# Optimization experiments

Measured on AMD Instinct MI355X. Metric: run time of the kernel, lower is better.

The kernel has to match this reference:

```python
import math
import jax, jax.numpy as jnp
import numpy as np

B, LD, LS = 1, 512, 2048
C_S, C_H, H, PQ, PV = 384, 16, 12, 4, 8
EPS, INF = 1e-08, 1e9


def _quat_to_rot(q):
    q = q / jnp.linalg.norm(q, axis=-1, keepdims=True)
    w, x, y, z = q[..., 0], q[..., 1], q[..., 2], q[..., 3]
    R = jnp.stack([
        1 - 2 * (y * y + z * z), 2 * (x * y - w * z), 2 * (x * z + w * y),
        2 * (x * y + w * z), 1 - 2 * (x * x + z * z), 2 * (y * z - w * x),
        2 * (x * z - w * y), 2 * (y * z + w * x), 1 - 2 * (x * x + y * y)],
        axis=-1)
    return R.reshape(q.shape[:-1] + (3, 3))


def setup_inputs() -> dict:
    key = jax.random.key(0)
    ks = jax.random.split(key, 14)
    s_dst = jax.random.normal(ks[0], (B, LD, C_S), jnp.float32)
    s_src = jax.random.normal(ks[1], (B, LS, C_S), jnp.float32)
    R_dst = _quat_to_rot(jax.random.normal(ks[2], (B, LD, 4), jnp.float32))
    t_dst = jax.random.normal(ks[3], (B, LD, 3), jnp.float32) * 3.0
    R_src = _quat_to_rot(jax.random.normal(ks[4], (B, LS, 4), jnp.float32))
    t_src = jax.random.normal(ks[5], (B, LS, 3), jnp.float32) * 3.0
    dst_mask = jnp.ones((B, LD), jnp.float32)
    src_mask = (jax.random.uniform(ks[6], (B, LS)) < 0.9).astype(jnp.float32)
    sc = 0.02
    W_q = jax.random.normal(ks[7], (C_S, H * C_H), jnp.float32) * sc
    W_kv = jax.random.normal(ks[8], (C_S, 2 * H * C_H), jnp.float32) * sc
    W_qp = jax.random.normal(ks[9], (C_S, H * PQ * 3), jnp.float32) * sc
    W_kvp = jax.random.normal(ks[10], (C_S, H * (PQ + PV) * 3), jnp.float32) * sc
    W_out = jax.random.normal(ks[11], (H * (C_H + PV * 4), C_S), jnp.float32) * sc
    b_out = jnp.zeros((C_S,), jnp.float32)
    # ipa_point_weights_init_: softplus^-1(1) = log(e - 1)
    head_w = jnp.full((H,), float(np.log(np.e - 1.0)), jnp.float32)
    return dict(s_dst=s_dst, s_src=s_src, R_dst=R_dst, t_dst=t_dst,
                R_src=R_src, t_src=t_src, dst_mask=dst_mask, src_mask=src_mask,
                W_q=W_q, W_kv=W_kv, W_qp=W_qp, W_kvp=W_kvp,
                W_out=W_out, b_out=b_out, head_w=head_w)


def _split3_stack(x):
    # torch.split into 3 chunks on last dim then stack(dim=-1): [..., 3n] -> [..., n, 3]
    b, l, c3 = x.shape
    return jnp.moveaxis(x.reshape(b, l, 3, c3 // 3), -2, -1)


def _ipa_forward(s_dst, s_src, R_dst, t_dst, R_src, t_src, dst_mask, src_mask,
                 W_q, W_kv, W_qp, W_kvp, W_out, b_out, head_w):
    b, ld, _ = s_dst.shape
    ls = s_src.shape[1]
    gmask = (dst_mask[:, None, :, None] * src_mask[:, None, None, :])  # [B,1,Ld,Ls]

    q = (s_dst @ W_q).reshape(b, ld, H, C_H)
    kv = (s_src @ W_kv).reshape(b, ls, H, 2 * C_H)
    k, v = kv[..., :C_H], kv[..., C_H:]

    # points in global frame
    qp = _split3_stack(s_dst @ W_qp)                     # [B,Ld,H*PQ,3] local
    qp = jnp.einsum('blij,blpj->blpi', R_dst, qp) + t_dst[:, :, None, :]
    qp = qp.reshape(b, ld, H, PQ, 3)
    kvp = _split3_stack(s_src @ W_kvp)                   # [B,Ls,H*(PQ+PV),3]
    kvp = jnp.einsum('blij,blpj->blpi', R_src, kvp) + t_src[:, :, None, :]
    kvp = kvp.reshape(b, ls, H, PQ + PV, 3)
    k_pts, v_pts = kvp[..., :PQ, :], kvp[..., PQ:, :]

    # scalar attention scores
    a = jnp.einsum('bihc,bjhc->bhij', q, k) * math.sqrt(1.0 / (2 * C_H))
    a_sd = a * gmask

    # point attention: squared distances of global-frame points
    diff = qp[:, :, None, :, :, :] - k_pts[:, None, :, :, :, :]   # [B,Ld,Ls,H,PQ,3]
    pt2 = jnp.sum(diff * diff, axis=-1)                           # [B,Ld,Ls,H,PQ]
    hw = jax.nn.softplus(head_w) * math.sqrt(1.0 / (2 * (PQ * 9.0 / 2)))
    pt_att = jnp.sum(pt2 * hw[None, None, None, :, None], axis=-1) * (-0.5)
    pt_att = jnp.transpose(pt_att, (0, 3, 1, 2))                  # [B,H,Ld,Ls]
    a_pts = pt_att * gmask

    sq_mask = INF * (dst_mask[:, :, None] * src_mask[:, None, :] - 1.0)
    a = jax.nn.softmax(a + pt_att + sq_mask[:, None, :, :], axis=-1)

    # scalar value aggregation
    o = jnp.einsum('bhij,bjhc->bihc', a, v).reshape(b, ld, H * C_H)
    # point value aggregation, then back to dst local frame
    o_pt = jnp.einsum('bhij,bjhpc->bihpc', a, v_pts)              # [B,Ld,H,PV,3]
    o_pt = jnp.einsum('bikj,bihpk->bihpj', R_dst,
                      o_pt - t_dst[:, :, None, None, :])
    o_pt_norm = jnp.sqrt(jnp.sum(o_pt ** 2, axis=-1) + EPS).reshape(b, ld, H * PV)
    o_pt_flat = o_pt.reshape(b, ld, H * PV, 3)

    cat = jnp.concatenate([o, o_pt_flat[..., 0], o_pt_flat[..., 1],
                           o_pt_flat[..., 2], o_pt_norm], axis=-1)
    s_upd = cat @ W_out + b_out
    return s_upd, a, a_sd, a_pts


def reference(s_dst, s_src, R_dst, t_dst, R_src, t_src, dst_mask, src_mask,
              W_q, W_kv, W_qp, W_kvp, W_out, b_out, head_w):
    return _ipa_forward(s_dst, s_src, R_dst, t_dst, R_src, t_src,
                        dst_mask, src_mask, W_q, W_kv, W_qp, W_kvp,
                        W_out, b_out, head_w)
```

## Files before the change

kernel.cpp:

```cpp
#include <hip/hip_runtime.h>
#include <hip/hip_bf16.h>

#define LD 512
#define LS 2048
#define CS 384
#define CH 16
#define NH 12
#define PQ 4
#define PV 8
#define QCW 336
#define KVW 816

typedef __bf16 bf16x8 __attribute__((ext_vector_type(8)));
typedef float  f32x4  __attribute__((ext_vector_type(4)));

__device__ inline void split_frag(const float* __restrict__ p, bf16x8& hi, bf16x8& lo)
{
    float4 x = *(const float4*)p;
    float4 y = *(const float4*)(p + 4);
    float f[8] = {x.x, x.y, x.z, x.w, y.x, y.y, y.z, y.w};
#pragma unroll
    for (int e = 0; e < 8; ++e) {
        __bf16 h = (__bf16)f[e];
        hi[e] = h;
        lo[e] = (__bf16)(f[e] - (float)h);
    }
}

__global__ __launch_bounds__(256) void transpose_w_all_kernel(
    const float* __restrict__ W_q, const float* __restrict__ W_kv,
    const float* __restrict__ W_qp, const float* __restrict__ W_kvp,
    const float* __restrict__ W_out,
    float* __restrict__ Wt_qc, float* __restrict__ Wt_kvc,
    float* __restrict__ Wt_out)
{
    int b = blockIdx.x;
    const float* src; float* dst; int R, Cc, gx;
    if (b < 72)       {         src = W_q;   dst = Wt_qc;             R = 384; Cc = 192; gx = 12; }
    else if (b < 132) { b -= 72;  src = W_qp;  dst = Wt_qc + 192*384; R = 384; Cc = 144; gx = 12; }
    else if (b < 276) { b -= 132; src = W_kv;  dst = Wt_kvc;          R = 384; Cc = 384; gx = 12; }
    else if (b < 444) { b -= 276; src = W_kvp; dst = Wt_kvc + 384*384;R = 384; Cc = 432; gx = 12; }
    else              { b -= 444; src = W_out; dst = Wt_out;          R = 576; Cc = 384; gx = 18; }
    const int r0 = (b % gx) * 32, c0 = (b / gx) * 32;

    __shared__ float tile[32][33];
    const int tx = threadIdx.x & 31, ty = threadIdx.x >> 5;
#pragma unroll
    for (int rr = 0; rr < 32; rr += 8) {
        int r = r0 + ty + rr, c = c0 + tx;
        tile[ty + rr][tx] = (r < R && c < Cc) ? src[(size_t)r * Cc + c] : 0.f;
    }
    __syncthreads();
#pragma unroll
    for (int rr = 0; rr < 32; rr += 8) {
        int c = c0 + ty + rr, r = r0 + tx;
        if (c < Cc && r < R) dst[(size_t)c * R + r] = tile[tx][ty + rr];
    }
}

__global__ __launch_bounds__(64) void mfma_gemm_bt_kernel(
    const float* __restrict__ A, const float* __restrict__ Bt,
    const float* __restrict__ bias, float* __restrict__ C,
    int M, int N, int K)
{
    const int m0 = blockIdx.x * 32;
    const int n0 = blockIdx.y * 32;
    const int lane = threadIdx.x;
    const int row16 = lane & 15, kq = lane >> 4;

    const float* ap0 = A + (size_t)(m0 + row16) * K + kq * 8;
    const float* ap1 = ap0 + (size_t)16 * K;
    const float* bp0 = Bt + (size_t)(n0 + row16) * K + kq * 8;
    const float* bp1 = bp0 + (size_t)16 * K;
    const bool n1ok = (n0 + 16) < N;

    f32x4 acc00 = {0.f, 0.f, 0.f, 0.f};
    f32x4 acc10 = {0.f, 0.f, 0.f, 0.f};
    f32x4 acc01 = {0.f, 0.f, 0.f, 0.f};
    f32x4 acc11 = {0.f, 0.f, 0.f, 0.f};

    for (int k = 0; k < K; k += 32) {
        bf16x8 a0h, a0l, a1h, a1l, b0h, b0l, b1h, b1l;
        split_frag(ap0 + k, a0h, a0l);
        split_frag(ap1 + k, a1h, a1l);
        split_frag(bp0 + k, b0h, b0l);
        acc00 = __builtin_amdgcn_mfma_f32_16x16x32_bf16(a0h, b0h, acc00, 0, 0, 0);
        acc00 = __builtin_amdgcn_mfma_f32_16x16x32_bf16(a0h, b0l, acc00, 0, 0, 0);
        acc00 = __builtin_amdgcn_mfma_f32_16x16x32_bf16(a0l, b0h, acc00, 0, 0, 0);
        acc10 = __builtin_amdgcn_mfma_f32_16x16x32_bf16(a1h, b0h, acc10, 0, 0, 0);
        acc10 = __builtin_amdgcn_mfma_f32_16x16x32_bf16(a1h, b0l, acc10, 0, 0, 0);
        acc10 = __builtin_amdgcn_mfma_f32_16x16x32_bf16(a1l, b0h, acc10, 0, 0, 0);
        if (n1ok) {
            split_frag(bp1 + k, b1h, b1l);
            acc01 = __builtin_amdgcn_mfma_f32_16x16x32_bf16(a0h, b1h, acc01, 0, 0, 0);
            acc01 = __builtin_amdgcn_mfma_f32_16x16x32_bf16(a0h, b1l, acc01, 0, 0, 0);
            acc01 = __builtin_amdgcn_mfma_f32_16x16x32_bf16(a0l, b1h, acc01, 0, 0, 0);
            acc11 = __builtin_amdgcn_mfma_f32_16x16x32_bf16(a1h, b1h, acc11, 0, 0, 0);
            acc11 = __builtin_amdgcn_mfma_f32_16x16x32_bf16(a1h, b1l, acc11, 0, 0, 0);
            acc11 = __builtin_amdgcn_mfma_f32_16x16x32_bf16(a1l, b1h, acc11, 0, 0, 0);
        }
    }

    const float bv0 = bias ? bias[n0 + row16] : 0.f;
    const float bv1 = (bias && n1ok) ? bias[n0 + 16 + row16] : 0.f;
#pragma unroll
    for (int r = 0; r < 4; ++r) {
        const int mA = m0 + kq * 4 + r;
        const int mB = mA + 16;
        C[(size_t)mA * N + n0 + row16] = acc00[r] + bv0;
        C[(size_t)mB * N + n0 + row16] = acc10[r] + bv0;
        if (n1ok) {
            C[(size_t)mA * N + n0 + 16 + row16] = acc01[r] + bv1;
            C[(size_t)mB * N + n0 + 16 + row16] = acc11[r] + bv1;
        }
    }
}

__global__ __launch_bounds__(256) void prep_kernel(
    const float* __restrict__ qcat, const float* __restrict__ kvcat,
    const float* __restrict__ Rd, const float* __restrict__ td,
    const float* __restrict__ Rs, const float* __restrict__ ts,
    float* __restrict__ qp_rot, float* __restrict__ sqq,
    float* __restrict__ kT, float* __restrict__ vAllT,
    float* __restrict__ kpT, float* __restrict__ sqkT)
{
    const int t = threadIdx.x;
    if (blockIdx.y < NH) {
        const int h = blockIdx.y, j0 = blockIdx.x * 64;
        __shared__ float tile[64][33];
        __shared__ float ot[36][64];
        __shared__ float nrm[64][4];
        __shared__ float rt[64][12];

#pragma unroll
        for (int s = 0; s < 3; ++s) {
            int ld = t + s * 256;
            int jl = ld / 12, q = ld % 12;
            rt[jl][q] = (q < 9) ? Rs[(size_t)(j0 + jl) * 9 + q]
                                : ts[(size_t)(j0 + jl) * 3 + (q - 9)];
        }
#pragma unroll
        for (int r = 0; r < 2; ++r) {
            int f = t + r * 256;
            int jl = f >> 3, c4 = (f & 7) * 4;
            float4 v = *(const float4*)(kvcat + (size_t)(j0 + jl) * KVW + h * 32 + c4);
            tile[jl][c4 + 0] = v.x;
            tile[jl][c4 + 1] = v.y;
            tile[jl][c4 + 2] = v.z;
            tile[jl][c4 + 3] = v.w;
        }
        __syncthreads();

        {
            const int jl = t & 63, cr = t >> 6;
#pragma unroll
            for (int cg = 0; cg < 8; ++cg) {
                int c = cg * 4 + cr;
                float v = tile[jl][c];
                if (c < 16) kT[((size_t)h * 16 + c) * LS + j0 + jl] = v;
                else        vAllT[((size_t)h * 40 + (c - 16)) * LS + j0 + jl] = v;
            }
        }

#pragma unroll
        for (int s = 0; s < 3; ++s) {
            int u = t + s * 256;
            int jl = u / 12, p = u % 12;
            const float* src = kvcat + (size_t)(j0 + jl) * KVW + 384 + h * 12 + p;
            float x = src[0], y = src[144], z = src[288];
            const float* R = &rt[jl][0];
            float rx = R[0] * x + R[1] * y + R[2] * z + R[9];
            float ry = R[3] * x + R[4] * y + R[5] * z + R[10];
            float rz = R[6] * x + R[7] * y + R[8] * z + R[11];
            if (p < 4) {
                ot[p * 3 + 0][jl] = rx;
                ot[p * 3 + 1][jl] = ry;
                ot[p * 3 + 2][jl] = rz;
                nrm[jl][p] = rx * rx + ry * ry + rz * rz;
            } else {
                int r0 = 12 + (p - 4) * 3;
                ot[r0 + 0][jl] = rx;
                ot[r0 + 1][jl] = ry;
                ot[r0 + 2][jl] = rz;
            }
        }
        __syncthreads();

#pragma unroll
        for (int w = 0; w < 9; ++w) {
            int idx = t + w * 256;
            int row = idx >> 6, jl = idx & 63;
            float v = ot[row][jl];
            if (row < 12) kpT[((size_t)h * 12 + row) * LS + j0 + jl] = v;
            else          vAllT[((size_t)h * 40 + 16 + (row - 12)) * LS + j0 + jl] = v;
        }
        if (t < 64)
            sqkT[(size_t)h * LS + j0 + t] = nrm[t][0] + nrm[t][1] + nrm[t][2] + nrm[t][3];
    } else {
        const int i0 = blockIdx.x * 16;
        __shared__ float part[16][48];
        __shared__ float rtd[16][12];
        if (t < 192) {
            int il = t / 12, q = t % 12;
            rtd[il][q] = (q < 9) ? Rd[(size_t)(i0 + il) * 9 + q]
                                 : td[(size_t)(i0 + il) * 3 + (q - 9)];
        }
        __syncthreads();
#pragma unroll
        for (int s = 0; s < 3; ++s) {
            int u = t + s * 256;
            int il = u / 48, pt = u % 48;
            int i = i0 + il;
            float x = qcat[(size_t)i * QCW + 192 + pt];
            float y = qcat[(size_t)i * QCW + 240 + pt];
            float z = qcat[(size_t)i * QCW + 288 + pt];
            const float* R = &rtd[il][0];
            float rx = R[0] * x + R[1] * y + R[2] * z + R[9];
            float ry = R[3] * x + R[4] * y + R[5] * z + R[10];
            float rz = R[6] * x + R[7] * y + R[8] * z + R[11];
            qp_rot[(size_t)i * 144 + pt * 3 + 0] = rx;
            qp_rot[(size_t)i * 144 + pt * 3 + 1] = ry;
            qp_rot[(size_t)i * 144 + pt * 3 + 2] = rz;
            part[il][pt] = rx * rx + ry * ry + rz * rz;
        }
        __syncthreads();
        if (t < 192) {
            int il = t / 12, hh = t % 12;
            sqq[(size_t)(i0 + il) * NH + hh] =
                part[il][hh * 4] + part[il][hh * 4 + 1] +
                part[il][hh * 4 + 2] + part[il][hh * 4 + 3];
        }
    }
}

__global__ __launch_bounds__(256) void score_softmax_kernel(
    const float* __restrict__ qb, const float* __restrict__ kT,
    const float* __restrict__ qpb, const float* __restrict__ kpT,
    const float* __restrict__ sqq_g, const float* __restrict__ sqkT,
    const float* __restrict__ dmask, const float* __restrict__ smask,
    const float* __restrict__ head_w,
    float* __restrict__ a_out, float* __restrict__ asd_out,
    float* __restrict__ apts_out)
{
    const int h = blockIdx.y;
    const int i0 = blockIdx.x * 4;
    const int t = threadIdx.x;

    __shared__ float qs[4][32];
    __shared__ float sqq_s[4];
    __shared__ float dm_s[4];
    __shared__ float red[4][4];

    if (t < 128) {
        int i = t >> 5, c = t & 31;
        float v = 0.f;
        if (c < 16)      v = qb[(size_t)(i0 + i) * QCW + h * CH + c];
        else if (c < 28) v = qpb[(size_t)(i0 + i) * 144 + h * 12 + (c - 16)];
        qs[i][c] = v;
    } else if (t < 132) {
        int i = t - 128;
        sqq_s[i] = sqq_g[(size_t)(i0 + i) * NH + h];
        dm_s[i] = dmask[i0 + i];
    }
    const float hwv = log1pf(__expf(head_w[h])) * (1.0f / 6.0f);
    const float s1 = 0.17677669529663687f;
    const size_t rowbase = ((size_t)h * LD + i0) * LS;
    __syncthreads();

    float4 sregv[4][2];
    float mx[4] = {-3.0e38f, -3.0e38f, -3.0e38f, -3.0e38f};

#pragma unroll
    for (int jc = 0; jc < 2; ++jc) {
        const int j = (jc * 256 + t) * 4;
        float4 sm4 = *(const float4*)(smask + j);
        float4 sqk4 = *(const float4*)(sqkT + (size_t)h * LS + j);

        float4 kk[16];
#pragma unroll
        for (int c = 0; c < 16; ++c)
            kk[c] = *(const float4*)(kT + ((size_t)h * 16 + c) * LS + j);

        float4 qk4[4];
#pragma unroll
        for (int i = 0; i < 4; ++i) {
            const float4* q4 = (const float4*)&qs[i][0];
            float4 q0 = q4[0], q1 = q4[1], q2 = q4[2], q3 = q4[3];
            float4 a;
            a.x = q0.x * kk[0].x + q0.y * kk[1].x + q0.z * kk[2].x + q0.w * kk[3].x
                + q1.x * kk[4].x + q1.y * kk[5].x + q1.z * kk[6].x + q1.w * kk[7].x
                + q2.x * kk[8].x + q2.y * kk[9].x + q2.z * kk[10].x + q2.w * kk[11].x
                + q3.x * kk[12].x + q3.y * kk[13].x + q3.z * kk[14].x + q3.w * kk[15].x;
            a.y = q0.x * kk[0].y + q0.y * kk[1].y + q0.z * kk[2].y + q0.w * kk[3].y
                + q1.x * kk[4].y + q1.y * kk[5].y + q1.z * kk[6].y + q1.w * kk[7].y
                + q2.x * kk[8].y + q2.y * kk[9].y + q2.z * kk[10].y + q2.w * kk[11].y
                + q3.x * kk[12].y + q3.y * kk[13].y + q3.z * kk[14].y + q3.w * kk[15].y;
            a.z = q0.x * kk[0].z + q0.y * kk[1].z + q0.z * kk[2].z + q0.w * kk[3].z
                + q1.x * kk[4].z + q1.y * kk[5].z + q1.z * kk[6].z + q1.w * kk[7].z
                + q2.x * kk[8].z + q2.y * kk[9].z + q2.z * kk[10].z + q2.w * kk[11].z
                + q3.x * kk[12].z + q3.y * kk[13].z + q3.z * kk[14].z + q3.w * kk[15].z;
            a.w = q0.x * kk[0].w + q0.y * kk[1].w + q0.z * kk[2].w + q0.w * kk[3].w
                + q1.x * kk[4].w + q1.y * kk[5].w + q1.z * kk[6].w + q1.w * kk[7].w
                + q2.x * kk[8].w + q2.y * kk[9].w + q2.z * kk[10].w + q2.w * kk[11].w
                + q3.x * kk[12].w + q3.y * kk[13].w + q3.z * kk[14].w + q3.w * kk[15].w;
            qk4[i] = a;
        }

        float4 pp[12];
#pragma unroll
        for (int d = 0; d < 12; ++d)
            pp[d] = *(const float4*)(kpT + ((size_t)h * 12 + d) * LS + j);

        float4 dp4[4];
#pragma unroll
        for (int i = 0; i < 4; ++i) {
            const float4* r4 = (const float4*)&qs[i][16];
            float4 r0 = r4[0], r1 = r4[1], r2 = r4[2];
            float4 d;
            d.x = r0.x * pp[0].x + r0.y * pp[1].x + r0.z * pp[2].x + r0.w * pp[3].x
                + r1.x * pp[4].x + r1.y * pp[5].x + r1.z * pp[6].x + r1.w * pp[7].x
                + r2.x * pp[8].x + r2.y * pp[9].x + r2.z * pp[10].x + r2.w * pp[11].x;
            d.y = r0.x * pp[0].y + r0.y * pp[1].y + r0.z * pp[2].y + r0.w * pp[3].y
                + r1.x * pp[4].y + r1.y * pp[5].y + r1.z * pp[6].y + r1.w * pp[7].y
                + r2.x * pp[8].y + r2.y * pp[9].y + r2.z * pp[10].y + r2.w * pp[11].y;
            d.z = r0.x * pp[0].z + r0.y * pp[1].z + r0.z * pp[2].z + r0.w * pp[3].z
                + r1.x * pp[4].z + r1.y * pp[5].z + r1.z * pp[6].z + r1.w * pp[7].z
                + r2.x * pp[8].z + r2.y * pp[9].z + r2.z * pp[10].z + r2.w * pp[11].z;
            d.w = r0.x * pp[0].w + r0.y * pp[1].w + r0.z * pp[2].w + r0.w * pp[3].w
                + r1.x * pp[4].w + r1.y * pp[5].w + r1.z * pp[6].w + r1.w * pp[7].w
                + r2.x * pp[8].w + r2.y * pp[9].w + r2.z * pp[10].w + r2.w * pp[11].w;
            dp4[i] = d;
        }

#pragma unroll
        for (int i = 0; i < 4; ++i) {
            float sqq = sqq_s[i];
            float dm = dm_s[i];
            float4 qk, pt, g, logit;
            qk.x = qk4[i].x * s1; qk.y = qk4[i].y * s1;
            qk.z = qk4[i].z * s1; qk.w = qk4[i].w * s1;
            pt.x = -0.5f * hwv * (sqq + sqk4.x - 2.f * dp4[i].x);
            pt.y = -0.5f * hwv * (sqq + sqk4.y - 2.f * dp4[i].y);
            pt.z = -0.5f * hwv * (sqq + sqk4.z - 2.f * dp4[i].z);
            pt.w = -0.5f * hwv * (sqq + sqk4.w - 2.f * dp4[i].w);
            g.x = dm * sm4.x; g.y = dm * sm4.y; g.z = dm * sm4.z; g.w = dm * sm4.w;
            size_t idx = rowbase + (size_t)i * LS + j;
            f32x4 asd = {qk.x * g.x, qk.y * g.y, qk.z * g.z, qk.w * g.w};
            f32x4 apts = {pt.x * g.x, pt.y * g.y, pt.z * g.z, pt.w * g.w};
            __builtin_nontemporal_store(asd, (f32x4*)(asd_out + idx));
            __builtin_nontemporal_store(apts, (f32x4*)(apts_out + idx));
            logit.x = qk.x + pt.x + 1.0e9f * (g.x - 1.0f);
            logit.y = qk.y + pt.y + 1.0e9f * (g.y - 1.0f);
            logit.z = qk.z + pt.z + 1.0e9f * (g.z - 1.0f);
            logit.w = qk.w + pt.w + 1.0e9f * (g.w - 1.0f);
            sregv[i][jc] = logit;
            mx[i] = fmaxf(mx[i], fmaxf(fmaxf(logit.x, logit.y), fmaxf(logit.z, logit.w)));
        }
    }

    const int lane = t & 63, wid = t >> 6;
#pragma unroll
    for (int i = 0; i < 4; ++i) {
        float v = mx[i];
        for (int off = 32; off > 0; off >>= 1) v = fmaxf(v, __shfl_xor(v, off));
        if (lane == 0) red[wid][i] = v;
    }
    __syncthreads();
    float M[4], sum[4] = {0.f, 0.f, 0.f, 0.f};
#pragma unroll
    for (int i = 0; i < 4; ++i)
        M[i] = fmaxf(fmaxf(red[0][i], red[1][i]), fmaxf(red[2][i], red[3][i]));
    __syncthreads();

#pragma unroll
    for (int jc = 0; jc < 2; ++jc) {
#pragma unroll
        for (int i = 0; i < 4; ++i) {
            float4 e;
            e.x = __expf(sregv[i][jc].x - M[i]);
            e.y = __expf(sregv[i][jc].y - M[i]);
            e.z = __expf(sregv[i][jc].z - M[i]);
            e.w = __expf(sregv[i][jc].w - M[i]);
            sregv[i][jc] = e;
            sum[i] += e.x + e.y + e.z + e.w;
        }
    }
#pragma unroll
    for (int i = 0; i < 4; ++i) {
        float v = sum[i];
        for (int off = 32; off > 0; off >>= 1) v += __shfl_xor(v, off);
        if (lane == 0) red[wid][i] = v;
    }
    __syncthreads();
    float inv[4];
#pragma unroll
    for (int i = 0; i < 4; ++i)
        inv[i] = 1.0f / (red[0][i] + red[1][i] + red[2][i] + red[3][i]);

#pragma unroll
    for (int jc = 0; jc < 2; ++jc) {
        const int j = (jc * 256 + t) * 4;
#pragma unroll
        for (int i = 0; i < 4; ++i) {
            float4 e = sregv[i][jc];
            float4 o = make_float4(e.x * inv[i], e.y * inv[i], e.z * inv[i], e.w * inv[i]);
            *(float4*)(a_out + rowbase + (size_t)i * LS + j) = o;
        }
    }
}

__global__ __launch_bounds__(512) void av_mfma_kernel(
    const float* __restrict__ a, const float* __restrict__ vAllT,
    float* __restrict__ o_buf, float* __restrict__ opt_buf)
{
    const int m0 = blockIdx.x * 16;
    const int h  = blockIdx.y;
    const int t = threadIdx.x;
    const int lane = t & 63;
    const int wid  = t >> 6;
    const int row16 = lane & 15, kq = lane >> 4;

    const size_t kbase = (size_t)wid * 256 + kq * 8;
    const float* ap  = a     + ((size_t)h * LD + m0 + row16) * LS + kbase;
    const float* v0p = vAllT + ((size_t)h * 40 +  0 + row16) * LS + kbase;
    const float* v1p = vAllT + ((size_t)h * 40 + 16 + row16) * LS + kbase;
    const float* v2p = vAllT + ((size_t)h * 40 + 24 + row16) * LS + kbase;

    f32x4 acc0 = {0.f, 0.f, 0.f, 0.f};
    f32x4 acc1 = {0.f, 0.f, 0.f, 0.f};
    f32x4 acc2 = {0.f, 0.f, 0.f, 0.f};

#pragma unroll 2
    for (int kk = 0; kk < 256; kk += 32) {
        bf16x8 ah, al, bh, bl;
        split_frag(ap + kk, ah, al);

        split_frag(v0p + kk, bh, bl);
        acc0 = __builtin_amdgcn_mfma_f32_16x16x32_bf16(ah, bh, acc0, 0, 0, 0);
        acc0 = __builtin_amdgcn_mfma_f32_16x16x32_bf16(ah, bl, acc0, 0, 0, 0);
        acc0 = __builtin_amdgcn_mfma_f32_16x16x32_bf16(al, bh, acc0, 0, 0, 0);

        split_frag(v1p + kk, bh, bl);
        acc1 = __builtin_amdgcn_mfma_f32_16x16x32_bf16(ah, bh, acc1, 0, 0, 0);
        acc1 = __builtin_amdgcn_mfma_f32_16x16x32_bf16(ah, bl, acc1, 0, 0, 0);
        acc1 = __builtin_amdgcn_mfma_f32_16x16x32_bf16(al, bh, acc1, 0, 0, 0);

        split_frag(v2p + kk, bh, bl);
        acc2 = __builtin_amdgcn_mfma_f32_16x16x32_bf16(ah, bh, acc2, 0, 0, 0);
        acc2 = __builtin_amdgcn_mfma_f32_16x16x32_bf16(ah, bl, acc2, 0, 0, 0);
        acc2 = __builtin_amdgcn_mfma_f32_16x16x32_bf16(al, bh, acc2, 0, 0, 0);
    }

    __shared__ float red[8][64][13];
#pragma unroll
    for (int r = 0; r < 4; ++r) {
        red[wid][lane][r]     = acc0[r];
        red[wid][lane][4 + r] = acc1[r];
        red[wid][lane][8 + r] = acc2[r];
    }
    __syncthreads();

    if (wid == 0) {
        float s[12];
#pragma unroll
        for (int r = 0; r < 12; ++r) {
            float v = red[0][lane][r];
#pragma unroll
            for (int w = 1; w < 8; ++w) v += red[w][lane][r];
            s[r] = v;
        }
        const int ib = m0 + kq * 4;
#pragma unroll
        for (int r = 0; r < 4; ++r) {
            const int i = ib + r;
            o_buf[(size_t)i * 192 + h * 16 + row16] = s[r];
            opt_buf[(size_t)i * 288 + h * 24 + row16] = s[4 + r];
            if (row16 >= 8)
                opt_buf[(size_t)i * 288 + h * 24 + 8 + row16] = s[8 + r];
        }
    }
}

__global__ __launch_bounds__(192) void finalize_kernel(
    const float* __restrict__ o_buf, const float* __restrict__ opt_buf,
    const float* __restrict__ Rd, const float* __restrict__ td,
    float* __restrict__ cat)
{
    const int i = blockIdx.x, t = threadIdx.x;
    cat[i * 576 + t] = o_buf[i * 192 + t];
    if (t < 96) {
        const float* op = opt_buf + i * 288 + t * 3;
        float x = op[0] - td[i * 3 + 0];
        float y = op[1] - td[i * 3 + 1];
        float z = op[2] - td[i * 3 + 2];
        const float* R = Rd + i * 9;
        float rx = R[0] * x + R[3] * y + R[6] * z;
        float ry = R[1] * x + R[4] * y + R[7] * z;
        float rz = R[2] * x + R[5] * y + R[8] * z;
        float* cc = cat + i * 576 + 192;
        cc[t] = rx;
        cc[96 + t] = ry;
        cc[192 + t] = rz;
        cc[288 + t] = sqrtf(rx * rx + ry * ry + rz * rz + 1e-8f);
    }
}

extern "C" void kernel_launch(void* const* d_in, const int* in_sizes, int n_in,
                              void* d_out, int out_size, void* d_ws, size_t ws_size,
                              hipStream_t stream)
{
    (void)in_sizes; (void)n_in; (void)out_size; (void)ws_size;
    const float* s_dst    = (const float*)d_in[0];
    const float* s_src    = (const float*)d_in[1];
    const float* R_dst    = (const float*)d_in[2];
    const float* t_dst    = (const float*)d_in[3];
    const float* R_src    = (const float*)d_in[4];
    const float* t_src    = (const float*)d_in[5];
    const float* dst_mask = (const float*)d_in[6];
    const float* src_mask = (const float*)d_in[7];
    const float* W_q      = (const float*)d_in[8];
    const float* W_kv     = (const float*)d_in[9];
    const float* W_qp     = (const float*)d_in[10];
    const float* W_kvp    = (const float*)d_in[11];
    const float* W_out    = (const float*)d_in[12];
    const float* b_out    = (const float*)d_in[13];
    const float* head_w   = (const float*)d_in[14];

    float* ws = (float*)d_ws;
    float* qcat    = ws;
    float* kvcat   = qcat    + 172032;
    float* qp_rot  = kvcat   + 1671168;
    float* sq_q    = qp_rot  + 73728;
    float* o_buf   = sq_q    + 6144;
    float* opt_buf = o_buf   + 98304;
    float* cat_buf = opt_buf + 147456;
    float* kT      = cat_buf + 294912;
    float* vAllT   = kT      + 393216;
    float* kpT     = vAllT   + 983040;
    float* sqkT    = kpT     + 294912;
    float* Wt_qc   = sqkT    + 24576;
    float* Wt_kvc  = Wt_qc   + 129024;
    float* Wt_out  = Wt_kvc  + 313344;

    float* out_s    = (float*)d_out;
    float* out_a    = out_s    + 196608;
    float* out_asd  = out_a    + 12582912;
    float* out_apts = out_asd  + 12582912;

    transpose_w_all_kernel<<<dim3(660), dim3(256), 0, stream>>>(
        W_q, W_kv, W_qp, W_kvp, W_out, Wt_qc, Wt_kvc, Wt_out);
    mfma_gemm_bt_kernel<<<dim3(16, 11), dim3(64), 0, stream>>>(s_dst, Wt_qc,  nullptr, qcat,  LD, QCW, CS);
    mfma_gemm_bt_kernel<<<dim3(64, 26), dim3(64), 0, stream>>>(s_src, Wt_kvc, nullptr, kvcat, LS, KVW, CS);
    prep_kernel<<<dim3(32, 13), dim3(256), 0, stream>>>(
        qcat, kvcat, R_dst, t_dst, R_src, t_src,
        qp_rot, sq_q, kT, vAllT, kpT, sqkT);
    score_softmax_kernel<<<dim3(LD / 4, NH), dim3(256), 0, stream>>>(
        qcat, kT, qp_rot, kpT, sq_q, sqkT, dst_mask, src_mask, head_w,
        out_a, out_asd, out_apts);
    av_mfma_kernel<<<dim3(LD / 16, NH), dim3(512), 0, stream>>>(out_a, vAllT, o_buf, opt_buf);
    finalize_kernel<<<LD, 192, 0, stream>>>(o_buf, opt_buf, R_dst, t_dst, cat_buf);
    mfma_gemm_bt_kernel<<<dim3(16, 12), dim3(64), 0, stream>>>(cat_buf, Wt_out, b_out, out_s, LD, CS, 576);
}
```

Before: 305.8 us.

## Drop weight transpose kernel; read weights directly in fused projection GEMM

Removes the separate weight-transpose launch and instead loads the untransposed W matrices with strided per-lane reads inside the GEMMs. The q and kv projection GEMMs are merged into one launch that picks its A, W and output by block index. This cuts two launches and an extra pass over the weights through memory. In exchange, the B-fragment loads become 8 scalar strided loads per lane instead of two float4 loads, which may hurt load efficiency, though adjacent lanes still read adjacent columns.

```diff
diff --git a/kernel.cpp b/kernel.cpp
--- a/kernel.cpp
+++ b/kernel.cpp
@@ -27,51 +27,48 @@
     }
 }
 
-__global__ __launch_bounds__(256) void transpose_w_all_kernel(
-    const float* __restrict__ W_q, const float* __restrict__ W_kv,
-    const float* __restrict__ W_qp, const float* __restrict__ W_kvp,
-    const float* __restrict__ W_out,
-    float* __restrict__ Wt_qc, float* __restrict__ Wt_kvc,
-    float* __restrict__ Wt_out)
-{
-    int b = blockIdx.x;
-    const float* src; float* dst; int R, Cc, gx;
-    if (b < 72)       {         src = W_q;   dst = Wt_qc;             R = 384; Cc = 192; gx = 12; }
-    else if (b < 132) { b -= 72;  src = W_qp;  dst = Wt_qc + 192*384; R = 384; Cc = 144; gx = 12; }
-    else if (b < 276) { b -= 132; src = W_kv;  dst = Wt_kvc;          R = 384; Cc = 384; gx = 12; }
-    else if (b < 444) { b -= 276; src = W_kvp; dst = Wt_kvc + 384*384;R = 384; Cc = 432; gx = 12; }
-    else              { b -= 444; src = W_out; dst = Wt_out;          R = 576; Cc = 384; gx = 18; }
-    const int r0 = (b % gx) * 32, c0 = (b / gx) * 32;
-
-    __shared__ float tile[32][33];
-    const int tx = threadIdx.x & 31, ty = threadIdx.x >> 5;
-#pragma unroll
-    for (int rr = 0; rr < 32; rr += 8) {
-        int r = r0 + ty + rr, c = c0 + tx;
-        tile[ty + rr][tx] = (r < R && c < Cc) ? src[(size_t)r * Cc + c] : 0.f;
-    }
-    __syncthreads();
-#pragma unroll
-    for (int rr = 0; rr < 32; rr += 8) {
-        int c = c0 + ty + rr, r = r0 + tx;
-        if (c < Cc && r < R) dst[(size_t)c * R + r] = tile[tx][ty + rr];
-    }
-}
-
-__global__ __launch_bounds__(64) void mfma_gemm_bt_kernel(
-    const float* __restrict__ A, const float* __restrict__ Bt,
-    const float* __restrict__ bias, float* __restrict__ C,
-    int M, int N, int K)
-{
-    const int m0 = blockIdx.x * 32;
-    const int n0 = blockIdx.y * 32;
+__device__ inline void split_frag_w(const float* __restrict__ Wp, int stride,
+                                    bf16x8& hi, bf16x8& lo)
+{
+    float f[8];
+#pragma unroll
+    for (int e = 0; e < 8; ++e) f[e] = Wp[(size_t)e * stride];
+#pragma unroll
+    for (int e = 0; e < 8; ++e) {
+        __bf16 h = (__bf16)f[e];
+        hi[e] = h;
+        lo[e] = (__bf16)(f[e] - (float)h);
+    }
+}
+
+__global__ __launch_bounds__(64) void proj_gemm_kernel(
+    const float* __restrict__ s_dst, const float* __restrict__ s_src,
+    const float* __restrict__ W_q, const float* __restrict__ W_qp,
+    const float* __restrict__ W_kv, const float* __restrict__ W_kvp,
+    float* __restrict__ qcat, float* __restrict__ kvcat)
+{
+    const float* A; float* C; int N, m0, n0, Nw; const float* Wsrc; int ncol0;
+    if (blockIdx.x < 176) {
+        int b = blockIdx.x;
+        A = s_dst; C = qcat; N = QCW;
+        m0 = (b & 15) * 32; n0 = (b >> 4) * 32;
+        if (n0 < 192) { Wsrc = W_q;  Nw = 192; ncol0 = n0; }
+        else          { Wsrc = W_qp; Nw = 144; ncol0 = n0 - 192; }
+    } else {
+        int b = blockIdx.x - 176;
+        A = s_src; C = kvcat; N = KVW;
+        m0 = (b & 63) * 32; n0 = (b >> 6) * 32;
+        if (n0 < 384) { Wsrc = W_kv;  Nw = 384; ncol0 = n0; }
+        else          { Wsrc = W_kvp; Nw = 432; ncol0 = n0 - 384; }
+    }
     const int lane = threadIdx.x;
     const int row16 = lane & 15, kq = lane >> 4;
+    const int K = CS;
 
     const float* ap0 = A + (size_t)(m0 + row16) * K + kq * 8;
     const float* ap1 = ap0 + (size_t)16 * K;
-    const float* bp0 = Bt + (size_t)(n0 + row16) * K + kq * 8;
-    const float* bp1 = bp0 + (size_t)16 * K;
+    const float* wp0 = Wsrc + (size_t)(kq * 8) * Nw + ncol0 + row16;
+    const float* wp1 = wp0 + 16;
     const bool n1ok = (n0 + 16) < N;
 
     f32x4 acc00 = {0.f, 0.f, 0.f, 0.f};
@@ -83,7 +80,7 @@
         bf16x8 a0h, a0l, a1h, a1l, b0h, b0l, b1h, b1l;
         split_frag(ap0 + k, a0h, a0l);
         split_frag(ap1 + k, a1h, a1l);
-        split_frag(bp0 + k, b0h, b0l);
+        split_frag_w(wp0 + (size_t)k * Nw, Nw, b0h, b0l);
         acc00 = __builtin_amdgcn_mfma_f32_16x16x32_bf16(a0h, b0h, acc00, 0, 0, 0);
         acc00 = __builtin_amdgcn_mfma_f32_16x16x32_bf16(a0h, b0l, acc00, 0, 0, 0);
         acc00 = __builtin_amdgcn_mfma_f32_16x16x32_bf16(a0l, b0h, acc00, 0, 0, 0);
@@ -91,7 +88,7 @@
         acc10 = __builtin_amdgcn_mfma_f32_16x16x32_bf16(a1h, b0l, acc10, 0, 0, 0);
         acc10 = __builtin_amdgcn_mfma_f32_16x16x32_bf16(a1l, b0h, acc10, 0, 0, 0);
         if (n1ok) {
-            split_frag(bp1 + k, b1h, b1l);
+            split_frag_w(wp1 + (size_t)k * Nw, Nw, b1h, b1l);
             acc01 = __builtin_amdgcn_mfma_f32_16x16x32_bf16(a0h, b1h, acc01, 0, 0, 0);
             acc01 = __builtin_amdgcn_mfma_f32_16x16x32_bf16(a0h, b1l, acc01, 0, 0, 0);
             acc01 = __builtin_amdgcn_mfma_f32_16x16x32_bf16(a0l, b1h, acc01, 0, 0, 0);
@@ -101,18 +98,69 @@
         }
     }
 
-    const float bv0 = bias ? bias[n0 + row16] : 0.f;
-    const float bv1 = (bias && n1ok) ? bias[n0 + 16 + row16] : 0.f;
+#pragma unroll
+    for (int r = 0; r < 4; ++r) {
+        const int mA = m0 + kq * 4 + r;
+        const int mB = mA + 16;
+        C[(size_t)mA * N + n0 + row16] = acc00[r];
+        C[(size_t)mB * N + n0 + row16] = acc10[r];
+        if (n1ok) {
+            C[(size_t)mA * N + n0 + 16 + row16] = acc01[r];
+            C[(size_t)mB * N + n0 + 16 + row16] = acc11[r];
+        }
+    }
+}
+
+__global__ __launch_bounds__(64) void out_gemm_kernel(
+    const float* __restrict__ A, const float* __restrict__ W_out,
+    const float* __restrict__ bias, float* __restrict__ C)
+{
+    const int m0 = blockIdx.x * 32;
+    const int n0 = blockIdx.y * 32;
+    const int lane = threadIdx.x;
+    const int row16 = lane & 15, kq = lane >> 4;
+    const int K = 576, N = CS, Nw = CS;
+
+    const float* ap0 = A + (size_t)(m0 + row16) * K + kq * 8;
+    const float* ap1 = ap0 + (size_t)16 * K;
+    const float* wp0 = W_out + (size_t)(kq * 8) * Nw + n0 + row16;
+    const float* wp1 = wp0 + 16;
+
+    f32x4 acc00 = {0.f, 0.f, 0.f, 0.f};
+    f32x4 acc10 = {0.f, 0.f, 0.f, 0.f};
+    f32x4 acc01 = {0.f, 0.f, 0.f, 0.f};
+    f32x4 acc11 = {0.f, 0.f, 0.f, 0.f};
+
+    for (int k = 0; k < K; k += 32) {
+        bf16x8 a0h, a0l, a1h, a1l, b0h, b0l, b1h, b1l;
+        split_frag(ap0 + k, a0h, a0l);
+        split_frag(ap1 + k, a1h, a1l);
+        split_frag_w(wp0 + (size_t)k * Nw, Nw, b0h, b0l);
+        acc00 = __builtin_amdgcn_mfma_f32_16x16x32_bf16(a0h, b0h, acc00, 0, 0, 0);
+        acc00 = __builtin_amdgcn_mfma_f32_16x16x32_bf16(a0h, b0l, acc00, 0, 0, 0);
+        acc00 = __builtin_amdgcn_mfma_f32_16x16x32_bf16(a0l, b0h, acc00, 0, 0, 0);
+        acc10 = __builtin_amdgcn_mfma_f32_16x16x32_bf16(a1h, b0h, acc10, 0, 0, 0);
+        acc10 = __builtin_amdgcn_mfma_f32_16x16x32_bf16(a1h, b0l, acc10, 0, 0, 0);
+        acc10 = __builtin_amdgcn_mfma_f32_16x16x32_bf16(a1l, b0h, acc10, 0, 0, 0);
+        split_frag_w(wp1 + (size_t)k * Nw, Nw, b1h, b1l);
+        acc01 = __builtin_amdgcn_mfma_f32_16x16x32_bf16(a0h, b1h, acc01, 0, 0, 0);
+        acc01 = __builtin_amdgcn_mfma_f32_16x16x32_bf16(a0h, b1l, acc01, 0, 0, 0);
+        acc01 = __builtin_amdgcn_mfma_f32_16x16x32_bf16(a0l, b1h, acc01, 0, 0, 0);
+        acc11 = __builtin_amdgcn_mfma_f32_16x16x32_bf16(a1h, b1h, acc11, 0, 0, 0);
+        acc11 = __builtin_amdgcn_mfma_f32_16x16x32_bf16(a1h, b1l, acc11, 0, 0, 0);
+        acc11 = __builtin_amdgcn_mfma_f32_16x16x32_bf16(a1l, b1h, acc11, 0, 0, 0);
+    }
+
+    const float bv0 = bias[n0 + row16];
+    const float bv1 = bias[n0 + 16 + row16];
 #pragma unroll
     for (int r = 0; r < 4; ++r) {
         const int mA = m0 + kq * 4 + r;
         const int mB = mA + 16;
         C[(size_t)mA * N + n0 + row16] = acc00[r] + bv0;
         C[(size_t)mB * N + n0 + row16] = acc10[r] + bv0;
-        if (n1ok) {
-            C[(size_t)mA * N + n0 + 16 + row16] = acc01[r] + bv1;
-            C[(size_t)mB * N + n0 + 16 + row16] = acc11[r] + bv1;
-        }
+        C[(size_t)mA * N + n0 + 16 + row16] = acc01[r] + bv1;
+        C[(size_t)mB * N + n0 + 16 + row16] = acc11[r] + bv1;
     }
 }
 
@@ -538,19 +586,14 @@
     float* vAllT   = kT      + 393216;
     float* kpT     = vAllT   + 983040;
     float* sqkT    = kpT     + 294912;
-    float* Wt_qc   = sqkT    + 24576;
-    float* Wt_kvc  = Wt_qc   + 129024;
-    float* Wt_out  = Wt_kvc  + 313344;
 
     float* out_s    = (float*)d_out;
     float* out_a    = out_s    + 196608;
     float* out_asd  = out_a    + 12582912;
     float* out_apts = out_asd  + 12582912;
 
-    transpose_w_all_kernel<<<dim3(660), dim3(256), 0, stream>>>(
-        W_q, W_kv, W_qp, W_kvp, W_out, Wt_qc, Wt_kvc, Wt_out);
-    mfma_gemm_bt_kernel<<<dim3(16, 11), dim3(64), 0, stream>>>(s_dst, Wt_qc,  nullptr, qcat,  LD, QCW, CS);
-    mfma_gemm_bt_kernel<<<dim3(64, 26), dim3(64), 0, stream>>>(s_src, Wt_kvc, nullptr, kvcat, LS, KVW, CS);
+    proj_gemm_kernel<<<dim3(1840), dim3(64), 0, stream>>>(
+        s_dst, s_src, W_q, W_qp, W_kv, W_kvp, qcat, kvcat);
     prep_kernel<<<dim3(32, 13), dim3(256), 0, stream>>>(
         qcat, kvcat, R_dst, t_dst, R_src, t_src,
         qp_rot, sq_q, kT, vAllT, kpT, sqkT);
@@ -559,5 +602,5 @@
         out_a, out_asd, out_apts);
     av_mfma_kernel<<<dim3(LD / 16, NH), dim3(512), 0, stream>>>(out_a, vAllT, o_buf, opt_buf);
     finalize_kernel<<<LD, 192, 0, stream>>>(o_buf, opt_buf, R_dst, t_dst, cat_buf);
-    mfma_gemm_bt_kernel<<<dim3(16, 12), dim3(64), 0, stream>>>(cat_buf, Wt_out, b_out, out_s, LD, CS, 576);
-}
+    out_gemm_kernel<<<dim3(16, 12), dim3(64), 0, stream>>>(cat_buf, W_out, b_out, out_s);
+}
```

Result: faster. 262.8 us (-14.1%).
